# Performance work log

Measured on AMD Instinct MI355X. Metric: run time of the kernel, lower is better.

The kernel has to match this reference:

```python
import jax, jax.numpy as jnp
import numpy as np

N, E = 50000, 800000
DIN, DH, DOUT, L = 128, 256, 64, 4


def setup_inputs() -> dict:
    key = jax.random.key(0)
    ks = jax.random.split(key, 8)
    x = jax.random.normal(ks[0], (N, DIN), dtype=jnp.float32)
    edge_index = jax.random.randint(ks[1], (2, E), 0, N, dtype=jnp.int64 if jax.config.jax_enable_x64 else jnp.int32)
    W_emb = jax.random.normal(ks[2], (DIN, DH), dtype=jnp.float32) / np.float32(np.sqrt(DIN))
    b_emb = jnp.zeros((DH,), jnp.float32)
    W_conv = jax.random.normal(ks[3], (L, DH, DH), dtype=jnp.float32) / np.float32(np.sqrt(DH))
    b_conv = jnp.zeros((L, DH), jnp.float32)
    W_out = jax.random.normal(ks[4], (DH, DOUT), dtype=jnp.float32) / np.float32(np.sqrt(DH))
    b_out = jnp.zeros((DOUT,), jnp.float32)
    return {"x": x, "edge_index": edge_index, "W_emb": W_emb, "b_emb": b_emb,
            "W_conv": W_conv, "b_conv": b_conv, "W_out": W_out, "b_out": b_out}


def _gcn_layer(h, src, dst, norm, W, b, n):
    # GCNConv: transform, then sym-normalized neighbor aggregation, then bias
    h = h @ W                                  # [N, DH]
    msg = h[src] * norm[:, None]               # [E+N, DH] gather + scale
    return jax.ops.segment_sum(msg, dst, num_segments=n) + b


def reference(x, edge_index, W_emb, b_emb, W_conv, b_conv, W_out, b_out):
    n = x.shape[0]
    loop = jnp.arange(n, dtype=edge_index.dtype)
    src = jnp.concatenate([edge_index[0], loop])   # add self-loops (PyG default)
    dst = jnp.concatenate([edge_index[1], loop])
    deg = jax.ops.segment_sum(jnp.ones_like(src, dtype=x.dtype), dst, num_segments=n)
    dinv = jnp.where(deg > 0, jax.lax.rsqrt(deg), jnp.zeros_like(deg))
    norm = dinv[src] * dinv[dst]                   # per-edge D^-1/2 A D^-1/2 weight
    h = x @ W_emb + b_emb                          # embedding (no activation)
    for i in range(L):                             # small fixed layer count
        h = jnp.tanh(_gcn_layer(h, src, dst, norm, W_conv[i], b_conv[i], n))
    return h @ W_out + b_out
```

## Files before the change

kernel.cpp:

```cpp
#include <hip/hip_runtime.h>
#include <math.h>

#define N_NODES 50000
#define N_EDGES 800000
#define DIN 128
#define DH 256
#define DOUT 64
#define NLAYERS 4

typedef unsigned short u16;
typedef __attribute__((ext_vector_type(8))) _Float16 half8;
typedef __attribute__((ext_vector_type(4))) float f32x4;

__device__ inline u16 f2h(float f) {
  _Float16 h = (_Float16)f;
  return *(u16*)&h;
}
__device__ inline float h2f(u16 u) {
  _Float16 h = *(_Float16*)&u;
  return (float)h;
}

#define GLD16(gp, lp)                                                        \
  __builtin_amdgcn_global_load_lds(                                          \
      (const __attribute__((address_space(1))) void*)(const void*)(gp),      \
      (__attribute__((address_space(3))) void*)(void*)(lp), 16, 0, 0)


__global__ void k_count(const int* __restrict__ dst, int* __restrict__ cnt, int e) {
  int i = blockIdx.x * blockDim.x + threadIdx.x;
  if (i < e) atomicAdd(&cnt[dst[i]], 1);
}

__global__ void k_scan1(const int* __restrict__ cnt, int* __restrict__ rowptr,
                        int* __restrict__ bsum, float* __restrict__ dinv, int n) {
  __shared__ int sm[256];
  int i = blockIdx.x * 256 + threadIdx.x;
  int v = (i < n) ? cnt[i] : 0;
  if (i < n) dinv[i] = rsqrtf((float)v + 1.0f);
  sm[threadIdx.x] = v;
  __syncthreads();
  for (int off = 1; off < 256; off <<= 1) {
    int t = (threadIdx.x >= off) ? sm[threadIdx.x - off] : 0;
    __syncthreads();
    sm[threadIdx.x] += t;
    __syncthreads();
  }
  if (i < n) rowptr[i + 1] = sm[threadIdx.x];
  if (threadIdx.x == 255) bsum[blockIdx.x] = sm[255];
}

__global__ void k_scan2(int* bsum, int nb) {
  __shared__ int sm[256];
  int v = (threadIdx.x < nb) ? bsum[threadIdx.x] : 0;
  sm[threadIdx.x] = v;
  __syncthreads();
  for (int off = 1; off < 256; off <<= 1) {
    int t = (threadIdx.x >= off) ? sm[threadIdx.x - off] : 0;
    __syncthreads();
    sm[threadIdx.x] += t;
    __syncthreads();
  }
  if (threadIdx.x < nb) bsum[threadIdx.x] = sm[threadIdx.x] - v;
}

__global__ void k_scan3(int* __restrict__ rowptr, const int* __restrict__ bsum,
                        int* __restrict__ cursor, int n) {
  int i = blockIdx.x * 256 + threadIdx.x;
  if (i < n) {
    int v = rowptr[i + 1] + bsum[blockIdx.x];
    rowptr[i + 1] = v;
    if (i + 1 < n) cursor[i + 1] = v;
  }
  if (blockIdx.x == 0 && threadIdx.x == 0) {
    rowptr[0] = 0;
    cursor[0] = 0;
  }
}

__global__ void k_fill(const int* __restrict__ src, const int* __restrict__ dst,
                       const float* __restrict__ dinv,
                       int* __restrict__ cursor, int2* __restrict__ csr, int e) {
  int i = blockIdx.x * blockDim.x + threadIdx.x;
  if (i < e) {
    int d = dst[i], s = src[i];
    int pos = atomicAdd(&cursor[d], 1);
    csr[pos] = make_int2(s, __float_as_int(dinv[s] * dinv[d]));
  }
}

#define X_Q (N_NODES * DIN / 4)
#define W_EMB_SZ (DIN * DH)
#define W_CONV_SZ (DH * DH)
#define W_OUT_SZ (3 * DH * DOUT)
#define W_TOT (W_EMB_SZ + 4 * W_CONV_SZ + W_OUT_SZ)

__global__ void k_convert(const float* __restrict__ x, u16* __restrict__ x_f16,
                          const float* __restrict__ W_emb, const float* __restrict__ W_conv,
                          const float* __restrict__ W_out, u16* __restrict__ Bt_emb,
                          u16* __restrict__ Bt_conv, u16* __restrict__ Bt_out) {
  int i = blockIdx.x * 256 + threadIdx.x;
  if (i < X_Q) {
    float4 v = ((const float4*)x)[i];
    ushort4 o;
    o.x = f2h(v.x); o.y = f2h(v.y); o.z = f2h(v.z); o.w = f2h(v.w);
    ((ushort4*)x_f16)[i] = o;
    return;
  }
  int t = i - X_Q;
  if (t < W_EMB_SZ) {
    int n = t >> 7, k = t & (DIN - 1);
    Bt_emb[t] = f2h(W_emb[k * DH + n]);
  } else if (t < W_EMB_SZ + 4 * W_CONV_SZ) {
    int j = t - W_EMB_SZ;
    int l = j >> 16, jj = j & (W_CONV_SZ - 1);
    int n = jj >> 8, k = jj & (DH - 1);
    Bt_conv[j] = f2h(W_conv[l * W_CONV_SZ + k * DH + n]);
  } else if (t < W_TOT) {
    int j = t - W_EMB_SZ - 4 * W_CONV_SZ;
    int n = j / (3 * DH), kp = j % (3 * DH);
    int k = (kp < DH) ? kp : ((kp < 2 * DH) ? kp - DH : kp - 2 * DH);
    float wv = W_out[k * DOUT + n];
    u16 hiv = f2h(wv);
    u16 v = hiv;
    if (kp >= DH && kp < 2 * DH) v = f2h(wv - h2f(hiv));
    Bt_out[j] = v;
  }
}

template <int BN, int NSPLIT, int EPI>
__global__ __launch_bounds__(256) void k_gemm_mfma(
    const u16* __restrict__ Ahi, const u16* __restrict__ Alo,
    const u16* __restrict__ Bt, const float* __restrict__ bias,
    float* __restrict__ Cf, u16* __restrict__ Cb, int M, int K, int N) {
  constexpr int BM = 128, BK = 64;
  constexpr int WN = BN / 2;
  constexpr int NT = WN / 16;
  constexpr int BNG = BN / 16;
  __shared__ u16 As[2 * 8 * 512];
  __shared__ u16 Bs[2 * BNG * 512];
  const int tid = threadIdx.x;
  const int w = tid >> 6, lane = tid & 63;
  const int q = lane >> 4, r = lane & 15;
  const int wmg = (w >> 1) * 4;
  const int wng = (w & 1) * NT;
  const int m0 = blockIdx.x * BM, n0 = blockIdx.y * BN;
  const int Kp = NSPLIT * K;
  const int srow = lane & 15;
  const int sk = (lane >> 4) * 8;

  f32x4 acc[4][NT];
#pragma unroll
  for (int t = 0; t < 4; t++)
#pragma unroll
    for (int u = 0; u < NT; u++) acc[t][u] = (f32x4){0.f, 0.f, 0.f, 0.f};

  for (int k0 = 0; k0 < Kp; k0 += BK) {
    const u16* Aptr;
    int ka;
    if (NSPLIT == 1) {
      Aptr = Ahi; ka = k0;
    } else {
      Aptr = (k0 < 2 * K) ? Ahi : Alo;
      ka = (k0 < K) ? k0 : ((k0 < 2 * K) ? (k0 - K) : (k0 - 2 * K));
    }
#pragma unroll
    for (int ii = 0; ii < 4; ii++) {
      int g = w * 2 + (ii & 1), kb = ii >> 1;
      int grow = m0 + g * 16 + srow;
      if (grow > M - 1) grow = M - 1;
      const u16* gp = Aptr + (size_t)grow * K + ka + kb * 32 + sk;
      GLD16(gp, &As[(kb * 8 + g) * 512] + (size_t)lane * 8);
    }
#pragma unroll
    for (int ii = 0; ii < BN / 32; ii++) {
      int g, kb;
      if (BN == 128) { g = w * 2 + (ii & 1); kb = ii >> 1; }
      else { g = w; kb = ii; }
      const u16* gp = Bt + (size_t)(n0 + g * 16 + srow) * Kp + k0 + kb * 32 + sk;
      GLD16(gp, &Bs[(kb * BNG + g) * 512] + (size_t)lane * 8);
    }
    __syncthreads();
#pragma unroll
    for (int kb = 0; kb < 2; kb++) {
      half8 af[4], bfr[NT];
#pragma unroll
      for (int t = 0; t < 4; t++)
        af[t] = *(const half8*)&As[((kb * 8 + wmg + t) * 64 + lane) * 8];
#pragma unroll
      for (int u = 0; u < NT; u++)
        bfr[u] = *(const half8*)&Bs[((kb * BNG + wng + u) * 64 + lane) * 8];
#pragma unroll
      for (int t = 0; t < 4; t++)
#pragma unroll
        for (int u = 0; u < NT; u++)
          acc[t][u] = __builtin_amdgcn_mfma_f32_16x16x32_f16(af[t], bfr[u], acc[t][u], 0, 0, 0);
    }
    __syncthreads();
  }

#pragma unroll
  for (int t = 0; t < 4; t++) {
#pragma unroll
    for (int rg = 0; rg < 4; rg++) {
      int row = m0 + (w >> 1) * 64 + t * 16 + q * 4 + rg;
      if (row < M) {
#pragma unroll
        for (int u = 0; u < NT; u++) {
          int col = n0 + (w & 1) * WN + u * 16 + r;
          float v = acc[t][u][rg];
          if (bias) v += bias[col];
          if (EPI == 0)
            Cf[(size_t)row * N + col] = v;
          else
            Cb[(size_t)row * N + col] = f2h(v);
        }
      }
    }
  }
}

__global__ void k_aggregate(const u16* __restrict__ tmph,
                            const int* __restrict__ rowptr, const int2* __restrict__ csr,
                            const float* __restrict__ dinv, const float* __restrict__ bias,
                            u16* __restrict__ hi, u16* __restrict__ lo, int n) {
  int i = (int)((blockIdx.x * (size_t)blockDim.x + threadIdx.x) >> 6);
  int lane = threadIdx.x & 63;
  if (i >= n) return;
  float w0 = dinv[i];
  w0 *= w0;
  const ushort4* T = (const ushort4*)tmph;
  float4 bv = ((const float4*)bias)[lane];
  ushort4 t0 = T[(size_t)i * 64 + lane];
  float ax = bv.x + w0 * h2f(t0.x);
  float ay = bv.y + w0 * h2f(t0.y);
  float az = bv.z + w0 * h2f(t0.z);
  float aw = bv.w + w0 * h2f(t0.w);
  int s = rowptr[i], e = rowptr[i + 1];
  int j = s;
  for (; j + 8 <= e; j += 8) {
    int2 c[8];
    ushort4 v[8];
#pragma unroll
    for (int u = 0; u < 8; u++) c[u] = csr[j + u];
#pragma unroll
    for (int u = 0; u < 8; u++) v[u] = T[(size_t)c[u].x * 64 + lane];
#pragma unroll
    for (int u = 0; u < 8; u++) {
      float f = __int_as_float(c[u].y);
      ax += f * h2f(v[u].x);
      ay += f * h2f(v[u].y);
      az += f * h2f(v[u].z);
      aw += f * h2f(v[u].w);
    }
  }
  for (; j + 4 <= e; j += 4) {
    int2 c[4];
    ushort4 v[4];
#pragma unroll
    for (int u = 0; u < 4; u++) c[u] = csr[j + u];
#pragma unroll
    for (int u = 0; u < 4; u++) v[u] = T[(size_t)c[u].x * 64 + lane];
#pragma unroll
    for (int u = 0; u < 4; u++) {
      float f = __int_as_float(c[u].y);
      ax += f * h2f(v[u].x);
      ay += f * h2f(v[u].y);
      az += f * h2f(v[u].z);
      aw += f * h2f(v[u].w);
    }
  }
  for (; j < e; j++) {
    int2 c = csr[j];
    ushort4 v = T[(size_t)c.x * 64 + lane];
    float f = __int_as_float(c.y);
    ax += f * h2f(v.x);
    ay += f * h2f(v.y);
    az += f * h2f(v.z);
    aw += f * h2f(v.w);
  }
  float ox = tanhf(ax), oy = tanhf(ay), oz = tanhf(az), ow = tanhf(aw);
  size_t base = (size_t)i * DH + lane * 4;
  ushort4 hv;
  hv.x = f2h(ox); hv.y = f2h(oy); hv.z = f2h(oz); hv.w = f2h(ow);
  *(ushort4*)(hi + base) = hv;
  if (lo) {
    ushort4 lv;
    lv.x = f2h(ox - h2f(hv.x));
    lv.y = f2h(oy - h2f(hv.y));
    lv.z = f2h(oz - h2f(hv.z));
    lv.w = f2h(ow - h2f(hv.w));
    *(ushort4*)(lo + base) = lv;
  }
}


extern "C" void kernel_launch(void* const* d_in, const int* in_sizes, int n_in,
                              void* d_out, int out_size, void* d_ws, size_t ws_size,
                              hipStream_t stream) {
  const float* x = (const float*)d_in[0];
  const int* eidx = (const int*)d_in[1];
  const int* esrc = eidx;
  const int* edst = eidx + N_EDGES;
  const float* W_emb = (const float*)d_in[2];
  const float* b_emb = (const float*)d_in[3];
  const float* W_conv = (const float*)d_in[4];
  const float* b_conv = (const float*)d_in[5];
  const float* W_out = (const float*)d_in[6];
  const float* b_out = (const float*)d_in[7];
  float* out = (float*)d_out;

  char* ws = (char*)d_ws;
  size_t off = 0;
  auto alloc = [&](size_t bytes) -> void* {
    void* p = ws + off;
    off += (bytes + 255) & ~(size_t)255;
    return p;
  };
  u16* tmph = (u16*)alloc((size_t)N_NODES * DH * 2);
  u16* h_hi = (u16*)alloc((size_t)N_NODES * DH * 2);
  u16* h_lo = (u16*)alloc((size_t)N_NODES * DH * 2);
  u16* x_f16 = h_lo;
  float* dinv = (float*)alloc((size_t)N_NODES * 4);
  int* cnt = (int*)alloc((size_t)N_NODES * 4);
  int* rowptr = (int*)alloc((size_t)(N_NODES + 1) * 4);
  int* cursor = (int*)alloc((size_t)N_NODES * 4);
  int* bsum = (int*)alloc((size_t)((N_NODES + 255) / 256) * 4);
  int2* csr = (int2*)alloc((size_t)N_EDGES * 8);
  u16* Bt_emb = (u16*)alloc((size_t)W_EMB_SZ * 2);
  u16* Bt_conv = (u16*)alloc((size_t)4 * W_CONV_SZ * 2);
  u16* Bt_out = (u16*)alloc((size_t)W_OUT_SZ * 2);

  int nb = (N_NODES + 255) / 256;
  int eb = (N_EDGES + 255) / 256;

  hipMemsetAsync(cnt, 0, (size_t)N_NODES * 4, stream);
  k_count<<<eb, 256, 0, stream>>>(edst, cnt, N_EDGES);
  k_scan1<<<nb, 256, 0, stream>>>(cnt, rowptr, bsum, dinv, N_NODES);
  k_scan2<<<1, 256, 0, stream>>>(bsum, nb);
  k_scan3<<<nb, 256, 0, stream>>>(rowptr, bsum, cursor, N_NODES);
  k_fill<<<eb, 256, 0, stream>>>(esrc, edst, dinv, cursor, csr, N_EDGES);
  k_convert<<<(X_Q + W_TOT + 255) / 256, 256, 0, stream>>>(x, x_f16, W_emb, W_conv, W_out,
                                                           Bt_emb, Bt_conv, Bt_out);

  int mblocks = (N_NODES + 127) / 128;
  int aggblocks = (N_NODES * 64 + 255) / 256;

  {
    dim3 g(mblocks, DH / 128);
    k_gemm_mfma<128, 1, 1><<<g, 256, 0, stream>>>(x_f16, nullptr, Bt_emb, b_emb,
                                                  nullptr, h_hi, N_NODES, DIN, DH);
  }
  for (int l = 0; l < NLAYERS; l++) {
    dim3 g(mblocks, DH / 128);
    k_gemm_mfma<128, 1, 1><<<g, 256, 0, stream>>>(h_hi, nullptr,
                                                  Bt_conv + (size_t)l * W_CONV_SZ, nullptr,
                                                  nullptr, tmph, N_NODES, DH, DH);
    k_aggregate<<<aggblocks, 256, 0, stream>>>(tmph, rowptr, csr, dinv,
                                               b_conv + (size_t)l * DH,
                                               h_hi, (l == 3) ? h_lo : nullptr, N_NODES);
  }
  {
    dim3 g(mblocks, 1);
    k_gemm_mfma<64, 3, 0><<<g, 256, 0, stream>>>(h_hi, h_lo, Bt_out, b_out,
                                                 out, nullptr, N_NODES, DH, DOUT);
  }
}
```

Before: 566.7 us.

## Permute hidden feature layout for vectorized GEMM stores, load B from global

The hidden-dimension columns are stored in a permuted order, so each lane's four MFMA output columns sit next to each other and the fp16 epilogue can write them as one ushort4 store instead of four scalar stores. Weights and biases are reindexed during conversion to match, which keeps the final output in its original order. B tiles are no longer staged through LDS; each lane reads its fragments straight from global/L2, which frees LDS but adds global load latency inside the MFMA loop. Edge-degree counting is also folded into the conversion kernel to save one launch.

```diff
diff --git a/kernel.cpp b/kernel.cpp
--- a/kernel.cpp
+++ b/kernel.cpp
@@ -20,17 +20,16 @@
   _Float16 h = *(_Float16*)&u;
   return (float)h;
 }
+__device__ inline int invp(int j) {
+  int s = j >> 6, t = j & 63;
+  return s * 64 + (t & 3) * 16 + (t >> 2);
+}
 
 #define GLD16(gp, lp)                                                        \
   __builtin_amdgcn_global_load_lds(                                          \
       (const __attribute__((address_space(1))) void*)(const void*)(gp),      \
       (__attribute__((address_space(3))) void*)(void*)(lp), 16, 0, 0)
 
-
-__global__ void k_count(const int* __restrict__ dst, int* __restrict__ cnt, int e) {
-  int i = blockIdx.x * blockDim.x + threadIdx.x;
-  if (i < e) atomicAdd(&cnt[dst[i]], 1);
-}
 
 __global__ void k_scan1(const int* __restrict__ cnt, int* __restrict__ rowptr,
                         int* __restrict__ bsum, float* __restrict__ dinv, int n) {
@@ -94,11 +93,16 @@
 #define W_CONV_SZ (DH * DH)
 #define W_OUT_SZ (3 * DH * DOUT)
 #define W_TOT (W_EMB_SZ + 4 * W_CONV_SZ + W_OUT_SZ)
+#define B_TOT (DH + 4 * DH)
 
 __global__ void k_convert(const float* __restrict__ x, u16* __restrict__ x_f16,
                           const float* __restrict__ W_emb, const float* __restrict__ W_conv,
-                          const float* __restrict__ W_out, u16* __restrict__ Bt_emb,
-                          u16* __restrict__ Bt_conv, u16* __restrict__ Bt_out) {
+                          const float* __restrict__ W_out,
+                          const float* __restrict__ b_emb, const float* __restrict__ b_conv,
+                          u16* __restrict__ Bt_emb, u16* __restrict__ Bt_conv,
+                          u16* __restrict__ Bt_out,
+                          float* __restrict__ bEmbP, float* __restrict__ bConvP,
+                          const int* __restrict__ edst, int* __restrict__ cnt) {
   int i = blockIdx.x * 256 + threadIdx.x;
   if (i < X_Q) {
     float4 v = ((const float4*)x)[i];
@@ -114,17 +118,29 @@
   } else if (t < W_EMB_SZ + 4 * W_CONV_SZ) {
     int j = t - W_EMB_SZ;
     int l = j >> 16, jj = j & (W_CONV_SZ - 1);
-    int n = jj >> 8, k = jj & (DH - 1);
-    Bt_conv[j] = f2h(W_conv[l * W_CONV_SZ + k * DH + n]);
+    int n = jj >> 8, k2 = jj & (DH - 1);
+    Bt_conv[j] = f2h(W_conv[l * W_CONV_SZ + invp(k2) * DH + n]);
   } else if (t < W_TOT) {
     int j = t - W_EMB_SZ - 4 * W_CONV_SZ;
     int n = j / (3 * DH), kp = j % (3 * DH);
-    int k = (kp < DH) ? kp : ((kp < 2 * DH) ? kp - DH : kp - 2 * DH);
-    float wv = W_out[k * DOUT + n];
+    int s0 = kp >> 8, k2 = kp & (DH - 1);
+    float wv = W_out[invp(k2) * DOUT + n];
     u16 hiv = f2h(wv);
     u16 v = hiv;
-    if (kp >= DH && kp < 2 * DH) v = f2h(wv - h2f(hiv));
+    if (s0 == 1) v = f2h(wv - h2f(hiv));
     Bt_out[j] = v;
+  } else {
+    int t2 = t - W_TOT;
+    if (t2 < B_TOT) {
+      if (t2 < DH) bEmbP[t2] = b_emb[invp(t2)];
+      else {
+        int j = t2 - DH, l = j >> 8, jj = j & (DH - 1);
+        bConvP[j] = b_conv[l * DH + invp(jj)];
+      }
+    } else {
+      int t3 = t2 - B_TOT;
+      if (t3 < N_EDGES) atomicAdd(&cnt[edst[t3]], 1);
+    }
   }
 }
 
@@ -136,14 +152,12 @@
   constexpr int BM = 128, BK = 64;
   constexpr int WN = BN / 2;
   constexpr int NT = WN / 16;
-  constexpr int BNG = BN / 16;
   __shared__ u16 As[2 * 8 * 512];
-  __shared__ u16 Bs[2 * BNG * 512];
   const int tid = threadIdx.x;
   const int w = tid >> 6, lane = tid & 63;
   const int q = lane >> 4, r = lane & 15;
   const int wmg = (w >> 1) * 4;
-  const int wng = (w & 1) * NT;
+  const int wn = (w & 1) * WN;
   const int m0 = blockIdx.x * BM, n0 = blockIdx.y * BN;
   const int Kp = NSPLIT * K;
   const int srow = lane & 15;
@@ -172,25 +186,18 @@
       const u16* gp = Aptr + (size_t)grow * K + ka + kb * 32 + sk;
       GLD16(gp, &As[(kb * 8 + g) * 512] + (size_t)lane * 8);
     }
-#pragma unroll
-    for (int ii = 0; ii < BN / 32; ii++) {
-      int g, kb;
-      if (BN == 128) { g = w * 2 + (ii & 1); kb = ii >> 1; }
-      else { g = w; kb = ii; }
-      const u16* gp = Bt + (size_t)(n0 + g * 16 + srow) * Kp + k0 + kb * 32 + sk;
-      GLD16(gp, &Bs[(kb * BNG + g) * 512] + (size_t)lane * 8);
-    }
     __syncthreads();
 #pragma unroll
     for (int kb = 0; kb < 2; kb++) {
       half8 af[4], bfr[NT];
 #pragma unroll
+      for (int u = 0; u < NT; u++)
+        bfr[u] = *(const half8*)(Bt + (size_t)(n0 + wn + u * 16 + r) * Kp +
+                                 k0 + kb * 32 + q * 8);
+#pragma unroll
       for (int t = 0; t < 4; t++)
         af[t] = *(const half8*)&As[((kb * 8 + wmg + t) * 64 + lane) * 8];
 #pragma unroll
-      for (int u = 0; u < NT; u++)
-        bfr[u] = *(const half8*)&Bs[((kb * BNG + wng + u) * 64 + lane) * 8];
-#pragma unroll
       for (int t = 0; t < 4; t++)
 #pragma unroll
         for (int u = 0; u < NT; u++)
@@ -199,21 +206,40 @@
     __syncthreads();
   }
 
-#pragma unroll
-  for (int t = 0; t < 4; t++) {
-#pragma unroll
-    for (int rg = 0; rg < 4; rg++) {
-      int row = m0 + (w >> 1) * 64 + t * 16 + q * 4 + rg;
-      if (row < M) {
-#pragma unroll
-        for (int u = 0; u < NT; u++) {
-          int col = n0 + (w & 1) * WN + u * 16 + r;
-          float v = acc[t][u][rg];
-          if (bias) v += bias[col];
-          if (EPI == 0)
-            Cf[(size_t)row * N + col] = v;
-          else
-            Cb[(size_t)row * N + col] = f2h(v);
+  if (EPI == 1) {
+    int cb = n0 + wn;
+    float4 bp = bias ? *(const float4*)(bias + cb + r * 4)
+                     : make_float4(0.f, 0.f, 0.f, 0.f);
+#pragma unroll
+    for (int t = 0; t < 4; t++) {
+#pragma unroll
+      for (int rg = 0; rg < 4; rg++) {
+        int row = m0 + (w >> 1) * 64 + t * 16 + q * 4 + rg;
+        if (row < M) {
+          ushort4 o;
+          o.x = f2h(acc[t][0][rg] + bp.x);
+          o.y = f2h(acc[t][1][rg] + bp.y);
+          o.z = f2h(acc[t][2][rg] + bp.z);
+          o.w = f2h(acc[t][3][rg] + bp.w);
+          *(ushort4*)(Cb + (size_t)row * N + cb + r * 4) = o;
+        }
+      }
+    }
+  } else {
+    float bv[NT];
+#pragma unroll
+    for (int u = 0; u < NT; u++) bv[u] = bias ? bias[n0 + wn + u * 16 + r] : 0.f;
+#pragma unroll
+    for (int t = 0; t < 4; t++) {
+#pragma unroll
+      for (int rg = 0; rg < 4; rg++) {
+        int row = m0 + (w >> 1) * 64 + t * 16 + q * 4 + rg;
+        if (row < M) {
+#pragma unroll
+          for (int u = 0; u < NT; u++) {
+            int col = n0 + wn + u * 16 + r;
+            Cf[(size_t)row * N + col] = acc[t][u][rg] + bv[u];
+          }
         }
       }
     }
@@ -330,25 +356,30 @@
   u16* Bt_emb = (u16*)alloc((size_t)W_EMB_SZ * 2);
   u16* Bt_conv = (u16*)alloc((size_t)4 * W_CONV_SZ * 2);
   u16* Bt_out = (u16*)alloc((size_t)W_OUT_SZ * 2);
+  float* bEmbP = (float*)alloc((size_t)DH * 4);
+  float* bConvP = (float*)alloc((size_t)4 * DH * 4);
 
   int nb = (N_NODES + 255) / 256;
   int eb = (N_EDGES + 255) / 256;
 
   hipMemsetAsync(cnt, 0, (size_t)N_NODES * 4, stream);
-  k_count<<<eb, 256, 0, stream>>>(edst, cnt, N_EDGES);
+  {
+    int tot = X_Q + W_TOT + B_TOT + N_EDGES;
+    k_convert<<<(tot + 255) / 256, 256, 0, stream>>>(x, x_f16, W_emb, W_conv, W_out,
+                                                     b_emb, b_conv, Bt_emb, Bt_conv,
+                                                     Bt_out, bEmbP, bConvP, edst, cnt);
+  }
   k_scan1<<<nb, 256, 0, stream>>>(cnt, rowptr, bsum, dinv, N_NODES);
   k_scan2<<<1, 256, 0, stream>>>(bsum, nb);
   k_scan3<<<nb, 256, 0, stream>>>(rowptr, bsum, cursor, N_NODES);
   k_fill<<<eb, 256, 0, stream>>>(esrc, edst, dinv, cursor, csr, N_EDGES);
-  k_convert<<<(X_Q + W_TOT + 255) / 256, 256, 0, stream>>>(x, x_f16, W_emb, W_conv, W_out,
-                                                           Bt_emb, Bt_conv, Bt_out);
 
   int mblocks = (N_NODES + 127) / 128;
   int aggblocks = (N_NODES * 64 + 255) / 256;
 
   {
     dim3 g(mblocks, DH / 128);
-    k_gemm_mfma<128, 1, 1><<<g, 256, 0, stream>>>(x_f16, nullptr, Bt_emb, b_emb,
+    k_gemm_mfma<128, 1, 1><<<g, 256, 0, stream>>>(x_f16, nullptr, Bt_emb, bEmbP,
                                                   nullptr, h_hi, N_NODES, DIN, DH);
   }
   for (int l = 0; l < NLAYERS; l++) {
@@ -357,7 +388,7 @@
                                                   Bt_conv + (size_t)l * W_CONV_SZ, nullptr,
                                                   nullptr, tmph, N_NODES, DH, DH);
     k_aggregate<<<aggblocks, 256, 0, stream>>>(tmph, rowptr, csr, dinv,
-                                               b_conv + (size_t)l * DH,
+                                               bConvP + (size_t)l * DH,
                                                h_hi, (l == 3) ? h_lo : nullptr, N_NODES);
   }
   {
```

Result: no change. 563.0 us (-0.7%).
